# Kernel optimization log

Measured on AMD Instinct MI355X. Metric: run time of the kernel, lower is better.

Reference implementation:

```python
import jax, jax.numpy as jnp
import numpy as np

B, N, CS, CZ, H, CH, G, P = 2, 384, 384, 128, 8, 16, 2, 8
CZ4 = CZ // 4
INF = 1e5
UMAX = 3.0     # self.u_max
LMAX = 2.0     # self.log_scale_max
SQRT_CH = CH ** 0.5


def quat_to_rot(q):
    q = q / jnp.linalg.norm(q, axis=-1, keepdims=True)
    w, x, y, z = q[..., 0], q[..., 1], q[..., 2], q[..., 3]
    R = jnp.stack([
        1 - 2 * (y * y + z * z), 2 * (x * y - w * z), 2 * (x * z + w * y),
        2 * (x * y + w * z), 1 - 2 * (x * x + z * z), 2 * (y * z - w * x),
        2 * (x * z - w * y), 2 * (y * z + w * x), 1 - 2 * (x * x + y * y)], axis=-1)
    return R.reshape(q.shape[:-1] + (3, 3))


def robust_nll(delta, sigma):
    # inline robust 3x3 Cholesky solve: dist_sq = d^T S^-1 d, log_det = ln|S|
    eps = 1e-8
    s00 = sigma[..., 0, 0]; s01 = sigma[..., 0, 1]; s02 = sigma[..., 0, 2]
    s11 = sigma[..., 1, 1]; s12 = sigma[..., 1, 2]; s22 = sigma[..., 2, 2]
    d0 = delta[..., 0]; d1 = delta[..., 1]; d2 = delta[..., 2]
    l00_sq = jnp.maximum(s00, eps); inv_l00 = jax.lax.rsqrt(l00_sq)
    l10 = s01 * inv_l00; l20 = s02 * inv_l00
    l11_sq = jnp.maximum(s11 - l10 * l10, eps); inv_l11 = jax.lax.rsqrt(l11_sq)
    l21 = (s12 - l20 * l10) * inv_l11
    l22_sq = jnp.maximum(s22 - l20 * l20 - l21 * l21, eps); inv_l22 = jax.lax.rsqrt(l22_sq)
    log_det = jnp.log(l00_sq) + jnp.log(l11_sq) + jnp.log(l22_sq)
    y0 = d0 * inv_l00
    y1 = (d1 - l10 * y0) * inv_l11
    y2 = (d2 - l20 * y0 - l21 * y1) * inv_l22
    return y0 * y0 + y1 * y1 + y2 * y2, log_det


def iga_forward(s, z, mask, rot, trans, local_mean, scaling_log,
                Wq, Wk, Wv, Wb, bb, Wdz, bdz, Wqg, bqg, Wkg, bkg,
                Wvp, bvp, geo_scale, geo_bias, Wout, bout):
    # scalar q/k/v: [B,H,N,CH]
    q = (s @ Wq).reshape(B, N, H, CH).transpose(0, 2, 1, 3)
    k = (s @ Wk).reshape(B, N, H, CH).transpose(0, 2, 1, 3)
    v = (s @ Wv).reshape(B, N, H, CH).transpose(0, 2, 1, 3)
    logits = jnp.einsum('bhid,bhjd->bhij', q, k) / SQRT_CH
    # pair bias: [B,H,N,N]
    logits = logits + (z @ Wb + bb).transpose(0, 3, 1, 2)

    def parse(feat):  # -> u [B,N,H,G,3], s_log_delta [B,N,H,G,3]
        raw = feat.reshape(B, N, H, G, 6)
        return jnp.tanh(raw[..., :3]) * UMAX, jnp.tanh(raw[..., 3:]) * LMAX

    def to_global(u, sld):
        anchor = local_mean[:, :, None, None, :]
        base = scaling_log[:, :, None, None, :]
        sig_loc = jnp.maximum(jnp.exp(base + sld), 1e-6)
        pos = anchor + u * sig_loc
        mu = jnp.einsum('bnij,bnhgj->bnhgi', rot, pos) + trans[:, :, None, None, :]
        var = jnp.exp(2.0 * (base + sld))
        Sig = jnp.einsum('bnij,bnhgj,bnkj->bnhgik', rot, var, rot)  # R diag(var) R^T
        return mu.transpose(0, 2, 1, 3, 4), Sig.transpose(0, 2, 1, 3, 4, 5)

    qu, qs = parse(s @ Wqg + bqg)
    ku, ks = parse(s @ Wkg + bkg)
    q_mu, q_sig = to_global(qu, qs)   # [B,H,N,G,3], [B,H,N,G,3,3]
    k_mu, k_sig = to_global(ku, ks)
    delta = q_mu[:, :, :, None] - k_mu[:, :, None, :]      # [B,H,N,N,G,3]
    ssum = q_sig[:, :, :, None] + k_sig[:, :, None, :]     # [B,H,N,N,G,3,3]
    dist_sq, log_det = robust_nll(delta, ssum)
    geo = (-0.5 * dist_sq - 0.5 * log_det).sum(-1)          # [B,H,N,N]

    mask2d = mask[:, None, :, None] * mask[:, None, None, :]  # [B,1,N,N]
    a = jax.nn.softplus(geo_scale)[None, :, None, None]
    G_geo = a * (geo * mask2d) + geo_bias[None, :, None, None]
    logits = logits + G_geo + (1.0 - mask2d) * (-INF)
    w = jax.nn.softmax(logits, axis=-1)                      # [B,H,N,N]

    # scalar output
    o = jnp.einsum('bhij,bhjd->bihd', w, v).reshape(B, N, H * CH)
    # point output (IPA-style): to global, attend, back to local frame
    vpts = (s @ Wvp + bvp).reshape(B, N, H, P, 3)
    vpg = jnp.einsum('bnij,bnhpj->bnhpi', rot, vpts) + trans[:, :, None, None, :]
    vpg = vpg.transpose(0, 2, 1, 3, 4)                       # [B,H,N,P,3]
    opt = jnp.einsum('bhij,bhjpc->bhipc', w, vpg)            # [B,H,N,P,3]
    opt_local = jnp.einsum('bnji,bhnpj->bnhpi', rot, opt - trans[:, None, :, None, :])
    onorm = jnp.sqrt((opt_local ** 2).sum(-1) + 1e-8)        # [B,N,H,P]
    # pair output
    pz = z @ Wdz + bdz                                       # [B,N,N,CZ4]
    opair = jnp.einsum('bhij,bijc->bihc', w, pz)             # [B,N,H,CZ4]

    cat = jnp.concatenate([o, opt_local.reshape(B, N, H * P * 3),
                           onorm.reshape(B, N, H * P),
                           opair.reshape(B, N, H * CZ4)], axis=-1)  # [B,N,640]
    return cat @ Wout + bout


def setup_inputs() -> dict:
    ks = jax.random.split(jax.random.key(0), 24)
    rnd = lambda i, shape, sc=1.0: jax.random.normal(ks[i], shape, dtype=jnp.float32) * sc
    w = 0.02
    return dict(
        s=rnd(0, (B, N, CS)), z=rnd(1, (B, N, N, CZ)),
        mask=jnp.ones((B, N), jnp.float32),
        rot=quat_to_rot(rnd(2, (B, N, 4))),
        trans=rnd(3, (B, N, 3), 1.0),
        local_mean=rnd(4, (B, N, 3), 0.5),
        scaling_log=rnd(5, (B, N, 3), 0.1),
        Wq=rnd(6, (CS, H * CH), w), Wk=rnd(7, (CS, H * CH), w), Wv=rnd(8, (CS, H * CH), w),
        Wb=rnd(9, (CZ, H), w), bb=rnd(10, (H,), w),
        Wdz=rnd(11, (CZ, CZ4), w), bdz=rnd(12, (CZ4,), w),
        Wqg=rnd(13, (CS, H * G * 6), w), bqg=rnd(14, (H * G * 6,), w),
        Wkg=rnd(15, (CS, H * G * 6), w), bkg=rnd(16, (H * G * 6,), w),
        Wvp=rnd(17, (CS, H * P * 3), w), bvp=rnd(18, (H * P * 3,), w),
        geo_scale=jnp.ones((H,), jnp.float32), geo_bias=jnp.zeros((H,), jnp.float32),
        Wout=rnd(19, (H * (CH + P * 4 + CZ4), CS), w), bout=jnp.zeros((CS,), jnp.float32))


def reference(s, z, mask, rot, trans, local_mean, scaling_log, Wq, Wk, Wv, Wb, bb,
              Wdz, bdz, Wqg, bqg, Wkg, bkg, Wvp, bvp, geo_scale, geo_bias, Wout, bout):
    return iga_forward(s, z, mask, rot, trans, local_mean, scaling_log, Wq, Wk, Wv,
                       Wb, bb, Wdz, bdz, Wqg, bqg, Wkg, bkg, Wvp, bvp,
                       geo_scale, geo_bias, Wout, bout)
```

## Files before the change

kernel.cpp:

```cpp
#include <hip/hip_runtime.h>
#include <hip/hip_fp16.h>

#define NB   2
#define NN   384
#define NCS  384
#define NCZ  128
#define NH   8
#define NCH  16
#define NG   2
#define NP   8
#define NCZ4 32
#define BN   (NB*NN)
#define LINW 768

typedef _Float16 f16x8 __attribute__((ext_vector_type(8)));
typedef float    f32x4 __attribute__((ext_vector_type(4)));

__global__ void k_wprep(const float* __restrict__ Wb, const float* __restrict__ Wdz,
                        _Float16* __restrict__ wf) {
    int t = threadIdx.x;
    for (int e = t; e < 12*64*8; e += 256) {
        int r = e & 7, lane = (e >> 3) & 63, nk = e >> 9;
        int n = nk >> 2, kk = nk & 3;
        int c = kk*32 + (lane >> 4)*8 + r;
        int col = n*16 + (lane & 15);
        float w;
        if      (col < 8)  w = Wb[c*NH + col];
        else if (col < 40) w = Wdz[c*NCZ4 + (col-8)];
        else               w = 0.f;
        wf[e] = (_Float16)w;
    }
}

__global__ void k_rowlin(const float* __restrict__ s,
                         const float* __restrict__ Wq, const float* __restrict__ Wk,
                         const float* __restrict__ Wv,
                         const float* __restrict__ Wqg, const float* __restrict__ bqg,
                         const float* __restrict__ Wkg, const float* __restrict__ bkg,
                         const float* __restrict__ Wvp, const float* __restrict__ bvp,
                         float* __restrict__ lin) {
    __shared__ float sl[4][NCS];
    int t  = threadIdx.x;
    int r0 = blockIdx.x * 4;
    for (int idx = t; idx < 4*NCS; idx += 256)
        sl[idx / NCS][idx % NCS] = s[(size_t)(r0 + idx/NCS)*NCS + (idx % NCS)];
    __syncthreads();
    int col = blockIdx.y * 256 + t;
    const float* W; int sw; float bias = 0.f;
    if      (col < 128) { W = Wq  + col;        sw = 128; }
    else if (col < 256) { W = Wk  + (col-128);  sw = 128; }
    else if (col < 384) { W = Wv  + (col-256);  sw = 128; }
    else if (col < 480) { W = Wqg + (col-384);  sw = 96;  bias = bqg[col-384]; }
    else if (col < 576) { W = Wkg + (col-480);  sw = 96;  bias = bkg[col-480]; }
    else                { W = Wvp + (col-576);  sw = 192; bias = bvp[col-576]; }
    float a0=0.f, a1=0.f, a2=0.f, a3=0.f;
    for (int c = 0; c < NCS; ++c) {
        float w = W[(size_t)c*sw];
        a0 = fmaf(sl[0][c], w, a0);
        a1 = fmaf(sl[1][c], w, a1);
        a2 = fmaf(sl[2][c], w, a2);
        a3 = fmaf(sl[3][c], w, a3);
    }
    lin[(size_t)(r0+0)*LINW + col] = a0 + bias;
    lin[(size_t)(r0+1)*LINW + col] = a1 + bias;
    lin[(size_t)(r0+2)*LINW + col] = a2 + bias;
    lin[(size_t)(r0+3)*LINW + col] = a3 + bias;
}

__global__ void k_geom(const float* __restrict__ lin, const float* __restrict__ rot,
                       const float* __restrict__ trans, const float* __restrict__ lm,
                       const float* __restrict__ sc,
                       float* __restrict__ qmu, float* __restrict__ qsig,
                       float* __restrict__ kmu, float* __restrict__ ksig,
                       float* __restrict__ vpg) {
    int bn = blockIdx.x, t = threadIdx.x;
    __shared__ float R[9], T[3], A[3], Bs[3];
    if (t < 9) R[t] = rot[bn*9 + t];
    if (t < 3) { T[t] = trans[bn*3+t]; A[t] = lm[bn*3+t]; Bs[t] = sc[bn*3+t]; }
    __syncthreads();
    {
        int h = t >> 3, p = t & 7;
        const float* vr = lin + (size_t)bn*LINW + 576 + h*24 + p*3;
        float x = vr[0], y = vr[1], z = vr[2];
        float* d = vpg + (size_t)bn*(NH*NP*3) + h*24 + p*3;
        d[0] = R[0]*x + R[1]*y + R[2]*z + T[0];
        d[1] = R[3]*x + R[4]*y + R[5]*z + T[1];
        d[2] = R[6]*x + R[7]*y + R[8]*z + T[2];
    }
    if (t < 32) {
        int side = t >> 4, item = t & 15;
        const float* raw = lin + (size_t)bn*LINW + (side ? 480 : 384) + item*6;
        float u0 = tanhf(raw[0])*3.f, u1 = tanhf(raw[1])*3.f, u2 = tanhf(raw[2])*3.f;
        float e0 = Bs[0] + tanhf(raw[3])*2.f;
        float e1 = Bs[1] + tanhf(raw[4])*2.f;
        float e2 = Bs[2] + tanhf(raw[5])*2.f;
        float sl0 = fmaxf(expf(e0), 1e-6f);
        float sl1 = fmaxf(expf(e1), 1e-6f);
        float sl2 = fmaxf(expf(e2), 1e-6f);
        float p0 = A[0] + u0*sl0, p1 = A[1] + u1*sl1, p2 = A[2] + u2*sl2;
        float mu0 = R[0]*p0 + R[1]*p1 + R[2]*p2 + T[0];
        float mu1 = R[3]*p0 + R[4]*p1 + R[5]*p2 + T[1];
        float mu2 = R[6]*p0 + R[7]*p1 + R[8]*p2 + T[2];
        float v0 = expf(2.f*e0), v1 = expf(2.f*e1), v2 = expf(2.f*e2);
        float s00 = R[0]*R[0]*v0 + R[1]*R[1]*v1 + R[2]*R[2]*v2;
        float s01 = R[0]*R[3]*v0 + R[1]*R[4]*v1 + R[2]*R[5]*v2;
        float s02 = R[0]*R[6]*v0 + R[1]*R[7]*v1 + R[2]*R[8]*v2;
        float s11 = R[3]*R[3]*v0 + R[4]*R[4]*v1 + R[5]*R[5]*v2;
        float s12 = R[3]*R[6]*v0 + R[4]*R[7]*v1 + R[5]*R[8]*v2;
        float s22 = R[6]*R[6]*v0 + R[7]*R[7]*v1 + R[8]*R[8]*v2;
        float* mud = (side ? kmu : qmu) + (size_t)bn*48 + item*3;
        mud[0]=mu0; mud[1]=mu1; mud[2]=mu2;
        float* sgd = (side ? ksig : qsig) + (size_t)bn*96 + item*6;
        sgd[0]=s00; sgd[1]=s01; sgd[2]=s02; sgd[3]=s11; sgd[4]=s12; sgd[5]=s22;
    }
}

__global__ void __launch_bounds__(256, 2)
k_attn(const float* __restrict__ z, const float* __restrict__ mask,
       const float* __restrict__ rot, const float* __restrict__ trans,
       const float* __restrict__ lin,
       const float* __restrict__ qmu, const float* __restrict__ qsig,
       const float* __restrict__ kmu, const float* __restrict__ ksig,
       const float* __restrict__ vpg, const _Float16* __restrict__ wf,
       const float* __restrict__ bb, const float* __restrict__ bdz,
       const float* __restrict__ gsc, const float* __restrict__ gbi,
       float* __restrict__ cat) {
    __shared__ __align__(16) _Float16 zh[64*128];
    __shared__ float  logits[NH][NN];
    __shared__ __half pzl[NN][34];
    __shared__ float  qrow[128];
    __shared__ float  qmu_s[48], qsig_s[96];
    __shared__ float  Rm[9], Tv[3];
    __shared__ float  aH[NH], bH[NH];
    __shared__ float  bias_s[48];
    __shared__ float  maskI;

    int t  = threadIdx.x;
    int lane = t & 63, w = t >> 6;
    int b  = blockIdx.x / NN, i = blockIdx.x % NN;
    int bi = b*NN + i;
    const float* zbase = z + (size_t)bi*NN*NCZ;

    const float* zrow0 = zbase + (size_t)(t >> 5)*NCZ + (t & 31)*4;
    float4 preA[8], preB[8];
    #pragma unroll
    for (int p = 0; p < 8; ++p) preA[p] = *(const float4*)(zrow0 + (size_t)(p*8)*NCZ);
    #pragma unroll
    for (int p = 0; p < 8; ++p) preB[p] = *(const float4*)(zrow0 + (size_t)(64 + p*8)*NCZ);

    f16x8 bfr[12];
    #pragma unroll
    for (int nk = 0; nk < 12; ++nk)
        bfr[nk] = ((const f16x8*)wf)[nk*64 + lane];

    if (t < 128) qrow[t] = lin[(size_t)bi*LINW + t];
    if (t < 48)  qmu_s[t] = qmu[(size_t)bi*48 + t];
    if (t < 48)  bias_s[t] = (t < 8) ? bb[t] : ((t < 40) ? bdz[t-8] : 0.f);
    if (t >= 64 && t < 160) qsig_s[t-64] = qsig[(size_t)bi*96 + (t-64)];
    if (t >= 160 && t < 169) Rm[t-160] = rot[bi*9 + (t-160)];
    if (t >= 169 && t < 172) Tv[t-169] = trans[bi*3 + (t-169)];
    if (t >= 176 && t < 184) {
        int h = t-176;
        float x = gsc[h];
        aH[h] = (x > 20.f) ? x : log1pf(expf(x));
        bH[h] = gbi[h];
    }
    if (t == 255) maskI = mask[bi];
    __syncthreads();

    {
        int h = t >> 5, lnn = t & 31;
        float qv[16];
        #pragma unroll
        for (int d = 0; d < 16; ++d) qv[d] = qrow[h*16 + d];
        float qm[6], qs[12];
        #pragma unroll
        for (int e = 0; e < 6; ++e)  qm[e] = qmu_s[h*6 + e];
        #pragma unroll
        for (int e = 0; e < 12; ++e) qs[e] = qsig_s[h*12 + e];
        float ascale = aH[h], hbias = bH[h], mI = maskI;
        for (int jj = 0; jj < 12; ++jj) {
            int j = lnn + jj*32;
            size_t jrow = (size_t)(b*NN + j);
            const float* kp = lin + jrow*LINW + 128 + h*NCH;
            float4 k0 = *(const float4*)(kp);
            float4 k1 = *(const float4*)(kp+4);
            float4 k2 = *(const float4*)(kp+8);
            float4 k3 = *(const float4*)(kp+12);
            float qk = qv[0]*k0.x + qv[1]*k0.y + qv[2]*k0.z + qv[3]*k0.w
                     + qv[4]*k1.x + qv[5]*k1.y + qv[6]*k1.z + qv[7]*k1.w
                     + qv[8]*k2.x + qv[9]*k2.y + qv[10]*k2.z + qv[11]*k2.w
                     + qv[12]*k3.x + qv[13]*k3.y + qv[14]*k3.z + qv[15]*k3.w;
            float geo = 0.f;
            #pragma unroll
            for (int g = 0; g < NG; ++g) {
                const float* km = kmu + jrow*48 + h*6 + g*3;
                const float* ks = ksig + jrow*96 + h*12 + g*6;
                float d0 = qm[g*3+0] - km[0];
                float d1 = qm[g*3+1] - km[1];
                float d2 = qm[g*3+2] - km[2];
                float s00 = qs[g*6+0] + ks[0];
                float s01 = qs[g*6+1] + ks[1];
                float s02 = qs[g*6+2] + ks[2];
                float s11 = qs[g*6+3] + ks[3];
                float s12 = qs[g*6+4] + ks[4];
                float s22 = qs[g*6+5] + ks[5];
                float l00 = fmaxf(s00, 1e-8f);
                float i00 = rsqrtf(l00);
                float l10 = s01*i00, l20 = s02*i00;
                float l11 = fmaxf(s11 - l10*l10, 1e-8f);
                float i11 = rsqrtf(l11);
                float l21 = (s12 - l20*l10)*i11;
                float l22 = fmaxf(s22 - l20*l20 - l21*l21, 1e-8f);
                float i22 = rsqrtf(l22);
                float ld = __logf(l00) + __logf(l11) + __logf(l22);
                float y0 = d0*i00;
                float y1 = (d1 - l10*y0)*i11;
                float y2 = (d2 - l20*y0 - l21*y1)*i22;
                geo += -0.5f*(y0*y0 + y1*y1 + y2*y2 + ld);
            }
            float m2 = mI * mask[b*NN + j];
            logits[h][j] = qk*0.25f + ascale*(geo*m2) + hbias + (1.f - m2)*(-100000.f);
        }
    }

    int srow0 = t >> 5;
    int scb   = (t & 31) * 8;
    int sswz  = (srow0 & 7) << 4;
    int arow  = w*16 + (lane & 15);
    int abase = arow*256 + ((lane >> 4) << 4);
    int akey  = (lane & 7) << 4;
    int ccol  = lane & 15;
    int cjl   = w*16 + (lane >> 4)*4;

#define CHUNK_BODY(CH, PRE)                                                          \
    {                                                                                \
                              \
        _Pragma("unroll")                                                            \
        for (int p = 0; p < 8; ++p) {                                                \
            union { _Float16 h[4]; unsigned long long u; } pk;                       \
            pk.h[0] = (_Float16)PRE[p].x; pk.h[1] = (_Float16)PRE[p].y;              \
            pk.h[2] = (_Float16)PRE[p].z; pk.h[3] = (_Float16)PRE[p].w;              \
            *(unsigned long long*)((char*)zh + (p*8 + srow0)*256 + (scb ^ sswz)) = pk.u; \
        }                                                                            \
        if ((CH) + 2 < 6) {         \
            const float* src = zbase + (size_t)((CH+2)*64)*NCZ + (size_t)(t>>5)*NCZ  \
                               + (t & 31)*4;                                         \
            _Pragma("unroll")                                                        \
            for (int p = 0; p < 8; ++p)                                              \
                PRE[p] = *(const float4*)(src + (size_t)(p*8)*NCZ);                  \
        }                                                                            \
        __syncthreads();                                                             \
        {                                                                            \
            f16x8 af0 = *(const f16x8*)((const char*)zh + ((abase +   0) ^ akey));   \
            f16x8 af1 = *(const f16x8*)((const char*)zh + ((abase +  64) ^ akey));   \
            f16x8 af2 = *(const f16x8*)((const char*)zh + ((abase + 128) ^ akey));   \
            f16x8 af3 = *(const f16x8*)((const char*)zh + ((abase + 192) ^ akey));   \
            f32x4 ac0 = {0.f,0.f,0.f,0.f}, ac1 = ac0, ac2 = ac0;                     \
            ac0 = __builtin_amdgcn_mfma_f32_16x16x32_f16(af0, bfr[0], ac0, 0,0,0);   \
            ac1 = __builtin_amdgcn_mfma_f32_16x16x32_f16(af0, bfr[4], ac1, 0,0,0);   \
            ac2 = __builtin_amdgcn_mfma_f32_16x16x32_f16(af0, bfr[8], ac2, 0,0,0);   \
            ac0 = __builtin_amdgcn_mfma_f32_16x16x32_f16(af1, bfr[1], ac0, 0,0,0);   \
            ac1 = __builtin_amdgcn_mfma_f32_16x16x32_f16(af1, bfr[5], ac1, 0,0,0);   \
            ac2 = __builtin_amdgcn_mfma_f32_16x16x32_f16(af1, bfr[9], ac2, 0,0,0);   \
            ac0 = __builtin_amdgcn_mfma_f32_16x16x32_f16(af2, bfr[2], ac0, 0,0,0);   \
            ac1 = __builtin_amdgcn_mfma_f32_16x16x32_f16(af2, bfr[6], ac1, 0,0,0);   \
            ac2 = __builtin_amdgcn_mfma_f32_16x16x32_f16(af2, bfr[10], ac2, 0,0,0);  \
            ac0 = __builtin_amdgcn_mfma_f32_16x16x32_f16(af3, bfr[3], ac0, 0,0,0);   \
            ac1 = __builtin_amdgcn_mfma_f32_16x16x32_f16(af3, bfr[7], ac1, 0,0,0);   \
            ac2 = __builtin_amdgcn_mfma_f32_16x16x32_f16(af3, bfr[11], ac2, 0,0,0);  \
            int jg = (CH)*64 + cjl;                                                  \
            _Pragma("unroll")                                                        \
            for (int r = 0; r < 4; ++r) {                                            \
                int j = jg + r;                                                      \
                float v0 = ac0[r] + bias_s[ccol];                                    \
                if (ccol < 8) logits[ccol][j] += v0;                                 \
                else          pzl[j][ccol-8] = __float2half(v0);                     \
                pzl[j][ccol+8] = __float2half(ac1[r] + bias_s[16+ccol]);             \
                if (ccol < 8)                                                        \
                    pzl[j][ccol+24] = __float2half(ac2[r] + bias_s[32+ccol]);        \
            }                                                                        \
        }                                                                            \
        __syncthreads();                                                             \
    }

    CHUNK_BODY(0, preA)
    CHUNK_BODY(1, preB)
    CHUNK_BODY(2, preA)
    CHUNK_BODY(3, preB)
    CHUNK_BODY(4, preA)
    CHUNK_BODY(5, preB)
#undef CHUNK_BODY

    int h = t >> 5, lnn = t & 31;
    float mx = -3.4e38f;
    #pragma unroll
    for (int jj = 0; jj < 12; ++jj) mx = fmaxf(mx, logits[h][lnn + jj*32]);
    #pragma unroll
    for (int m = 16; m >= 1; m >>= 1) mx = fmaxf(mx, __shfl_xor(mx, m, 64));
    float se = 0.f;
    #pragma unroll
    for (int jj = 0; jj < 12; ++jj) {
        int j = lnn + jj*32;
        float e = __expf(logits[h][j] - mx);
        logits[h][j] = e;
        se += e;
    }
    #pragma unroll
    for (int m = 16; m >= 1; m >>= 1) se += __shfl_xor(se, m, 64);
    float inv = 1.f / se;

    float o[16], op[24], opa[32];
    #pragma unroll
    for (int d = 0; d < 16; ++d) o[d] = 0.f;
    #pragma unroll
    for (int e = 0; e < 24; ++e) op[e] = 0.f;
    #pragma unroll
    for (int c = 0; c < 32; ++c) opa[c] = 0.f;

    for (int jj = 0; jj < 12; ++jj) {
        int j = lnn + jj*32;
        float wgt = logits[h][j] * inv;
        size_t jrow = (size_t)(b*NN + j);
        const float* vp = lin + jrow*LINW + 256 + h*NCH;
        float vv[16];
        *reinterpret_cast<float4*>(&vv[0])  = *(const float4*)(vp);
        *reinterpret_cast<float4*>(&vv[4])  = *(const float4*)(vp+4);
        *reinterpret_cast<float4*>(&vv[8])  = *(const float4*)(vp+8);
        *reinterpret_cast<float4*>(&vv[12]) = *(const float4*)(vp+12);
        #pragma unroll
        for (int d = 0; d < 16; ++d) o[d] = fmaf(wgt, vv[d], o[d]);
        const float* vg = vpg + jrow*(NH*NP*3) + h*24;
        float gg[24];
        #pragma unroll
        for (int q4 = 0; q4 < 6; ++q4)
            *reinterpret_cast<float4*>(&gg[q4*4]) = *(const float4*)(vg + q4*4);
        #pragma unroll
        for (int e = 0; e < 24; ++e) op[e] = fmaf(wgt, gg[e], op[e]);
        const __half2* pzp = reinterpret_cast<const __half2*>(&pzl[j][0]);
        #pragma unroll
        for (int c2 = 0; c2 < 16; ++c2) {
            float2 pf = __half22float2(pzp[c2]);
            opa[2*c2]   = fmaf(wgt, pf.x, opa[2*c2]);
            opa[2*c2+1] = fmaf(wgt, pf.y, opa[2*c2+1]);
        }
    }
    #pragma unroll
    for (int m = 16; m >= 1; m >>= 1) {
        #pragma unroll
        for (int d = 0; d < 16; ++d) o[d] += __shfl_xor(o[d], m, 64);
        #pragma unroll
        for (int e = 0; e < 24; ++e) op[e] += __shfl_xor(op[e], m, 64);
        #pragma unroll
        for (int c = 0; c < 32; ++c) opa[c] += __shfl_xor(opa[c], m, 64);
    }
    if (lnn == 0) {
        float* cp = cat + (size_t)bi*640;
        #pragma unroll
        for (int d = 0; d < 16; ++d) cp[h*16 + d] = o[d];
        #pragma unroll
        for (int p = 0; p < 8; ++p) {
            float x  = op[p*3+0] - Tv[0];
            float y  = op[p*3+1] - Tv[1];
            float zz = op[p*3+2] - Tv[2];
            float l0 = Rm[0]*x + Rm[3]*y + Rm[6]*zz;
            float l1 = Rm[1]*x + Rm[4]*y + Rm[7]*zz;
            float l2 = Rm[2]*x + Rm[5]*y + Rm[8]*zz;
            cp[128 + h*24 + p*3 + 0] = l0;
            cp[128 + h*24 + p*3 + 1] = l1;
            cp[128 + h*24 + p*3 + 2] = l2;
            cp[320 + h*8 + p] = sqrtf(l0*l0 + l1*l1 + l2*l2 + 1e-8f);
        }
        #pragma unroll
        for (int c = 0; c < 32; ++c) cp[384 + h*32 + c] = opa[c];
    }
}

__global__ void k_out(const float* __restrict__ cat, const float* __restrict__ Wout,
                      const float* __restrict__ bout, float* __restrict__ out) {
    __shared__ float cl[4][640];
    int t  = threadIdx.x;
    int r0 = blockIdx.x * 4;
    for (int idx = t; idx < 4*640; idx += 384)
        cl[idx/640][idx%640] = cat[(size_t)(r0 + idx/640)*640 + (idx%640)];
    __syncthreads();
    int col = t;
    float a0=0.f, a1=0.f, a2=0.f, a3=0.f;
    for (int c = 0; c < 640; ++c) {
        float w = Wout[(size_t)c*NCS + col];
        a0 = fmaf(cl[0][c], w, a0);
        a1 = fmaf(cl[1][c], w, a1);
        a2 = fmaf(cl[2][c], w, a2);
        a3 = fmaf(cl[3][c], w, a3);
    }
    float bv = bout[col];
    out[(size_t)(r0+0)*NCS + col] = a0 + bv;
    out[(size_t)(r0+1)*NCS + col] = a1 + bv;
    out[(size_t)(r0+2)*NCS + col] = a2 + bv;
    out[(size_t)(r0+3)*NCS + col] = a3 + bv;
}

extern "C" void kernel_launch(void* const* d_in, const int* in_sizes, int n_in,
                              void* d_out, int out_size, void* d_ws, size_t ws_size,
                              hipStream_t stream) {
    const float* s    = (const float*)d_in[0];
    const float* z    = (const float*)d_in[1];
    const float* mask = (const float*)d_in[2];
    const float* rot  = (const float*)d_in[3];
    const float* trans= (const float*)d_in[4];
    const float* lm   = (const float*)d_in[5];
    const float* sc   = (const float*)d_in[6];
    const float* Wq   = (const float*)d_in[7];
    const float* Wk   = (const float*)d_in[8];
    const float* Wv   = (const float*)d_in[9];
    const float* Wb   = (const float*)d_in[10];
    const float* bb   = (const float*)d_in[11];
    const float* Wdz  = (const float*)d_in[12];
    const float* bdz  = (const float*)d_in[13];
    const float* Wqg  = (const float*)d_in[14];
    const float* bqg  = (const float*)d_in[15];
    const float* Wkg  = (const float*)d_in[16];
    const float* bkg  = (const float*)d_in[17];
    const float* Wvp  = (const float*)d_in[18];
    const float* bvp  = (const float*)d_in[19];
    const float* gsc  = (const float*)d_in[20];
    const float* gbi  = (const float*)d_in[21];
    const float* Wout = (const float*)d_in[22];
    const float* bout = (const float*)d_in[23];
    float* out = (float*)d_out;

    float* ws   = (float*)d_ws;
    float* lin  = ws;
    float* qmu  = lin  + 589824;
    float* qsig = qmu  + 36864;
    float* kmu  = qsig + 73728;
    float* ksig = kmu  + 36864;
    float* vpg  = ksig + 73728;
    float* cat  = vpg  + 147456;
    _Float16* wf = (_Float16*)(cat + 491520);

    k_wprep<<<1, 256, 0, stream>>>(Wb, Wdz, wf);
    k_rowlin<<<dim3(192, 3), 256, 0, stream>>>(s, Wq, Wk, Wv, Wqg, bqg, Wkg, bkg,
                                               Wvp, bvp, lin);
    k_geom<<<BN, 64, 0, stream>>>(lin, rot, trans, lm, sc, qmu, qsig, kmu, ksig, vpg);
    k_attn<<<BN, 256, 0, stream>>>(z, mask, rot, trans, lin, qmu, qsig, kmu, ksig,
                                   vpg, wf, bb, bdz, gsc, gbi, cat);
    k_out<<<192, 384, 0, stream>>>(cat, Wout, bout, out);
}
```

Measured before the change: 180.1 us.

## Transpose key-side tensors to feature-major layout for coalesced attention loads

```diff
diff --git a/kernel.cpp b/kernel.cpp
--- a/kernel.cpp
+++ b/kernel.cpp
@@ -38,7 +38,8 @@
                          const float* __restrict__ Wqg, const float* __restrict__ bqg,
                          const float* __restrict__ Wkg, const float* __restrict__ bkg,
                          const float* __restrict__ Wvp, const float* __restrict__ bvp,
-                         float* __restrict__ lin) {
+                         float* __restrict__ lin,
+                         float* __restrict__ kT, float* __restrict__ vT) {
     __shared__ float sl[4][NCS];
     int t  = threadIdx.x;
     int r0 = blockIdx.x * 4;
@@ -65,14 +66,20 @@
     lin[(size_t)(r0+1)*LINW + col] = a1 + bias;
     lin[(size_t)(r0+2)*LINW + col] = a2 + bias;
     lin[(size_t)(r0+3)*LINW + col] = a3 + bias;
+    if (col >= 128 && col < 384) {
+        f32x4 v4; v4[0]=a0; v4[1]=a1; v4[2]=a2; v4[3]=a3;
+        float* dst = (col < 256) ? (kT + (size_t)(col-128)*BN + r0)
+                                 : (vT + (size_t)(col-256)*BN + r0);
+        *(f32x4*)dst = v4;
+    }
 }
 
 __global__ void k_geom(const float* __restrict__ lin, const float* __restrict__ rot,
                        const float* __restrict__ trans, const float* __restrict__ lm,
                        const float* __restrict__ sc,
                        float* __restrict__ qmu, float* __restrict__ qsig,
-                       float* __restrict__ kmu, float* __restrict__ ksig,
-                       float* __restrict__ vpg) {
+                       float* __restrict__ kmuT, float* __restrict__ ksigT,
+                       float* __restrict__ vpgT) {
     int bn = blockIdx.x, t = threadIdx.x;
     __shared__ float R[9], T[3], A[3], Bs[3];
     if (t < 9) R[t] = rot[bn*9 + t];
@@ -82,10 +89,10 @@
         int h = t >> 3, p = t & 7;
         const float* vr = lin + (size_t)bn*LINW + 576 + h*24 + p*3;
         float x = vr[0], y = vr[1], z = vr[2];
-        float* d = vpg + (size_t)bn*(NH*NP*3) + h*24 + p*3;
-        d[0] = R[0]*x + R[1]*y + R[2]*z + T[0];
-        d[1] = R[3]*x + R[4]*y + R[5]*z + T[1];
-        d[2] = R[6]*x + R[7]*y + R[8]*z + T[2];
+        int e = h*24 + p*3;
+        vpgT[(size_t)(e+0)*BN + bn] = R[0]*x + R[1]*y + R[2]*z + T[0];
+        vpgT[(size_t)(e+1)*BN + bn] = R[3]*x + R[4]*y + R[5]*z + T[1];
+        vpgT[(size_t)(e+2)*BN + bn] = R[6]*x + R[7]*y + R[8]*z + T[2];
     }
     if (t < 32) {
         int side = t >> 4, item = t & 15;
@@ -108,10 +115,22 @@
         float s11 = R[3]*R[3]*v0 + R[4]*R[4]*v1 + R[5]*R[5]*v2;
         float s12 = R[3]*R[6]*v0 + R[4]*R[7]*v1 + R[5]*R[8]*v2;
         float s22 = R[6]*R[6]*v0 + R[7]*R[7]*v1 + R[8]*R[8]*v2;
-        float* mud = (side ? kmu : qmu) + (size_t)bn*48 + item*3;
-        mud[0]=mu0; mud[1]=mu1; mud[2]=mu2;
-        float* sgd = (side ? ksig : qsig) + (size_t)bn*96 + item*6;
-        sgd[0]=s00; sgd[1]=s01; sgd[2]=s02; sgd[3]=s11; sgd[4]=s12; sgd[5]=s22;
+        if (side) {
+            kmuT[(size_t)(item*3+0)*BN + bn] = mu0;
+            kmuT[(size_t)(item*3+1)*BN + bn] = mu1;
+            kmuT[(size_t)(item*3+2)*BN + bn] = mu2;
+            ksigT[(size_t)(item*6+0)*BN + bn] = s00;
+            ksigT[(size_t)(item*6+1)*BN + bn] = s01;
+            ksigT[(size_t)(item*6+2)*BN + bn] = s02;
+            ksigT[(size_t)(item*6+3)*BN + bn] = s11;
+            ksigT[(size_t)(item*6+4)*BN + bn] = s12;
+            ksigT[(size_t)(item*6+5)*BN + bn] = s22;
+        } else {
+            float* mud = qmu + (size_t)bn*48 + item*3;
+            mud[0]=mu0; mud[1]=mu1; mud[2]=mu2;
+            float* sgd = qsig + (size_t)bn*96 + item*6;
+            sgd[0]=s00; sgd[1]=s01; sgd[2]=s02; sgd[3]=s11; sgd[4]=s12; sgd[5]=s22;
+        }
     }
 }
 
@@ -120,8 +139,9 @@
        const float* __restrict__ rot, const float* __restrict__ trans,
        const float* __restrict__ lin,
        const float* __restrict__ qmu, const float* __restrict__ qsig,
-       const float* __restrict__ kmu, const float* __restrict__ ksig,
-       const float* __restrict__ vpg, const _Float16* __restrict__ wf,
+       const float* __restrict__ kmuT, const float* __restrict__ ksigT,
+       const float* __restrict__ kT, const float* __restrict__ vT,
+       const float* __restrict__ vpgT, const _Float16* __restrict__ wf,
        const float* __restrict__ bb, const float* __restrict__ bdz,
        const float* __restrict__ gsc, const float* __restrict__ gbi,
        float* __restrict__ cat) {
@@ -140,6 +160,7 @@
     int b  = blockIdx.x / NN, i = blockIdx.x % NN;
     int bi = b*NN + i;
     const float* zbase = z + (size_t)bi*NN*NCZ;
+    const size_t boff = (size_t)b*NN;
 
     const float* zrow0 = zbase + (size_t)(t >> 5)*NCZ + (t & 31)*4;
     float4 preA[8], preB[8];
@@ -147,11 +168,6 @@
     for (int p = 0; p < 8; ++p) preA[p] = *(const float4*)(zrow0 + (size_t)(p*8)*NCZ);
     #pragma unroll
     for (int p = 0; p < 8; ++p) preB[p] = *(const float4*)(zrow0 + (size_t)(64 + p*8)*NCZ);
-
-    f16x8 bfr[12];
-    #pragma unroll
-    for (int nk = 0; nk < 12; ++nk)
-        bfr[nk] = ((const f16x8*)wf)[nk*64 + lane];
 
     if (t < 128) qrow[t] = lin[(size_t)bi*LINW + t];
     if (t < 48)  qmu_s[t] = qmu[(size_t)bi*48 + t];
@@ -179,50 +195,72 @@
         #pragma unroll
         for (int e = 0; e < 12; ++e) qs[e] = qsig_s[h*12 + e];
         float ascale = aH[h], hbias = bH[h], mI = maskI;
-        for (int jj = 0; jj < 12; ++jj) {
-            int j = lnn + jj*32;
-            size_t jrow = (size_t)(b*NN + j);
-            const float* kp = lin + jrow*LINW + 128 + h*NCH;
-            float4 k0 = *(const float4*)(kp);
-            float4 k1 = *(const float4*)(kp+4);
-            float4 k2 = *(const float4*)(kp+8);
-            float4 k3 = *(const float4*)(kp+12);
-            float qk = qv[0]*k0.x + qv[1]*k0.y + qv[2]*k0.z + qv[3]*k0.w
-                     + qv[4]*k1.x + qv[5]*k1.y + qv[6]*k1.z + qv[7]*k1.w
-                     + qv[8]*k2.x + qv[9]*k2.y + qv[10]*k2.z + qv[11]*k2.w
-                     + qv[12]*k3.x + qv[13]*k3.y + qv[14]*k3.z + qv[15]*k3.w;
-            float geo = 0.f;
+        #pragma unroll 1
+        for (int jj = 0; jj < 3; ++jj) {
+            int j4 = jj*128 + lnn*4;
+            const float* kp = kT + (size_t)(h*16)*BN + boff + j4;
+            f32x4 qk = {0.f,0.f,0.f,0.f};
+            #pragma unroll
+            for (int d = 0; d < 16; ++d) {
+                f32x4 kv = *(const f32x4*)(kp + (size_t)d*BN);
+                #pragma unroll
+                for (int r = 0; r < 4; ++r) qk[r] = fmaf(qv[d], kv[r], qk[r]);
+            }
+            f32x4 geo = {0.f,0.f,0.f,0.f};
             #pragma unroll
             for (int g = 0; g < NG; ++g) {
-                const float* km = kmu + jrow*48 + h*6 + g*3;
-                const float* ks = ksig + jrow*96 + h*12 + g*6;
-                float d0 = qm[g*3+0] - km[0];
-                float d1 = qm[g*3+1] - km[1];
-                float d2 = qm[g*3+2] - km[2];
-                float s00 = qs[g*6+0] + ks[0];
-                float s01 = qs[g*6+1] + ks[1];
-                float s02 = qs[g*6+2] + ks[2];
-                float s11 = qs[g*6+3] + ks[3];
-                float s12 = qs[g*6+4] + ks[4];
-                float s22 = qs[g*6+5] + ks[5];
-                float l00 = fmaxf(s00, 1e-8f);
-                float i00 = rsqrtf(l00);
-                float l10 = s01*i00, l20 = s02*i00;
-                float l11 = fmaxf(s11 - l10*l10, 1e-8f);
-                float i11 = rsqrtf(l11);
-                float l21 = (s12 - l20*l10)*i11;
-                float l22 = fmaxf(s22 - l20*l20 - l21*l21, 1e-8f);
-                float i22 = rsqrtf(l22);
-                float ld = __logf(l00) + __logf(l11) + __logf(l22);
-                float y0 = d0*i00;
-                float y1 = (d1 - l10*y0)*i11;
-                float y2 = (d2 - l20*y0 - l21*y1)*i22;
-                geo += -0.5f*(y0*y0 + y1*y1 + y2*y2 + ld);
+                const float* kmb = kmuT + (size_t)((h*2+g)*3)*BN + boff + j4;
+                f32x4 km0 = *(const f32x4*)(kmb);
+                f32x4 km1 = *(const f32x4*)(kmb + BN);
+                f32x4 km2 = *(const f32x4*)(kmb + 2*BN);
+                const float* ksb = ksigT + (size_t)((h*2+g)*6)*BN + boff + j4;
+                f32x4 ks0 = *(const f32x4*)(ksb);
+                f32x4 ks1 = *(const f32x4*)(ksb + BN);
+                f32x4 ks2 = *(const f32x4*)(ksb + 2*BN);
+                f32x4 ks3 = *(const f32x4*)(ksb + 3*BN);
+                f32x4 ks4 = *(const f32x4*)(ksb + 4*BN);
+                f32x4 ks5 = *(const f32x4*)(ksb + 5*BN);
+                #pragma unroll
+                for (int r = 0; r < 4; ++r) {
+                    float d0 = qm[g*3+0] - km0[r];
+                    float d1 = qm[g*3+1] - km1[r];
+                    float d2 = qm[g*3+2] - km2[r];
+                    float s00 = qs[g*6+0] + ks0[r];
+                    float s01 = qs[g*6+1] + ks1[r];
+                    float s02 = qs[g*6+2] + ks2[r];
+                    float s11 = qs[g*6+3] + ks3[r];
+                    float s12 = qs[g*6+4] + ks4[r];
+                    float s22 = qs[g*6+5] + ks5[r];
+                    float l00 = fmaxf(s00, 1e-8f);
+                    float i00 = rsqrtf(l00);
+                    float l10 = s01*i00, l20 = s02*i00;
+                    float l11 = fmaxf(s11 - l10*l10, 1e-8f);
+                    float i11 = rsqrtf(l11);
+                    float l21 = (s12 - l20*l10)*i11;
+                    float l22 = fmaxf(s22 - l20*l20 - l21*l21, 1e-8f);
+                    float i22 = rsqrtf(l22);
+                    float ld = __logf(l00) + __logf(l11) + __logf(l22);
+                    float y0 = d0*i00;
+                    float y1 = (d1 - l10*y0)*i11;
+                    float y2 = (d2 - l20*y0 - l21*y1)*i22;
+                    geo[r] += -0.5f*(y0*y0 + y1*y1 + y2*y2 + ld);
+                }
             }
-            float m2 = mI * mask[b*NN + j];
-            logits[h][j] = qk*0.25f + ascale*(geo*m2) + hbias + (1.f - m2)*(-100000.f);
+            f32x4 mv = *(const f32x4*)(mask + boff + j4);
+            f32x4 lg;
+            #pragma unroll
+            for (int r = 0; r < 4; ++r) {
+                float m2 = mI * mv[r];
+                lg[r] = qk[r]*0.25f + ascale*(geo[r]*m2) + hbias + (1.f - m2)*(-100000.f);
+            }
+            *(f32x4*)&logits[h][j4] = lg;
         }
     }
+
+    f16x8 bfr[12];
+    #pragma unroll
+    for (int nk = 0; nk < 12; ++nk)
+        bfr[nk] = ((const f16x8*)wf)[nk*64 + lane];
 
     int srow0 = t >> 5;
     int scb   = (t & 31) * 8;
@@ -235,7 +273,6 @@
 
 #define CHUNK_BODY(CH, PRE)                                                          \
     {                                                                                \
-                              \
         _Pragma("unroll")                                                            \
         for (int p = 0; p < 8; ++p) {                                                \
             union { _Float16 h[4]; unsigned long long u; } pk;                       \
@@ -243,7 +280,7 @@
             pk.h[2] = (_Float16)PRE[p].z; pk.h[3] = (_Float16)PRE[p].w;              \
             *(unsigned long long*)((char*)zh + (p*8 + srow0)*256 + (scb ^ sswz)) = pk.u; \
         }                                                                            \
-        if ((CH) + 2 < 6) {         \
+        if ((CH) + 2 < 6) {                                                          \
             const float* src = zbase + (size_t)((CH+2)*64)*NCZ + (size_t)(t>>5)*NCZ  \
                                + (t & 31)*4;                                         \
             _Pragma("unroll")                                                        \
@@ -318,25 +355,18 @@
     #pragma unroll
     for (int c = 0; c < 32; ++c) opa[c] = 0.f;
 
+    const float* vbase = vT + (size_t)(h*16)*BN + boff + lnn;
+    const float* gbase = vpgT + (size_t)(h*24)*BN + boff + lnn;
+    #pragma unroll 1
     for (int jj = 0; jj < 12; ++jj) {
         int j = lnn + jj*32;
         float wgt = logits[h][j] * inv;
-        size_t jrow = (size_t)(b*NN + j);
-        const float* vp = lin + jrow*LINW + 256 + h*NCH;
-        float vv[16];
-        *reinterpret_cast<float4*>(&vv[0])  = *(const float4*)(vp);
-        *reinterpret_cast<float4*>(&vv[4])  = *(const float4*)(vp+4);
-        *reinterpret_cast<float4*>(&vv[8])  = *(const float4*)(vp+8);
-        *reinterpret_cast<float4*>(&vv[12]) = *(const float4*)(vp+12);
-        #pragma unroll
-        for (int d = 0; d < 16; ++d) o[d] = fmaf(wgt, vv[d], o[d]);
-        const float* vg = vpg + jrow*(NH*NP*3) + h*24;
-        float gg[24];
-        #pragma unroll
-        for (int q4 = 0; q4 < 6; ++q4)
-            *reinterpret_cast<float4*>(&gg[q4*4]) = *(const float4*)(vg + q4*4);
-        #pragma unroll
-        for (int e = 0; e < 24; ++e) op[e] = fmaf(wgt, gg[e], op[e]);
+        const float* vb = vbase + jj*32;
+        #pragma unroll
+        for (int d = 0; d < 16; ++d) o[d] = fmaf(wgt, vb[(size_t)d*BN], o[d]);
+        const float* gb = gbase + jj*32;
+        #pragma unroll
+        for (int e = 0; e < 24; ++e) op[e] = fmaf(wgt, gb[(size_t)e*BN], op[e]);
         const __half2* pzp = reinterpret_cast<const __half2*>(&pzl[j][0]);
         #pragma unroll
         for (int c2 = 0; c2 < 16; ++c2) {
@@ -429,21 +459,23 @@
     const float* bout = (const float*)d_in[23];
     float* out = (float*)d_out;
 
-    float* ws   = (float*)d_ws;
-    float* lin  = ws;
-    float* qmu  = lin  + 589824;
-    float* qsig = qmu  + 36864;
-    float* kmu  = qsig + 73728;
-    float* ksig = kmu  + 36864;
-    float* vpg  = ksig + 73728;
-    float* cat  = vpg  + 147456;
+    float* ws    = (float*)d_ws;
+    float* lin   = ws;
+    float* qmu   = lin   + 589824;
+    float* qsig  = qmu   + 36864;
+    float* kmuT  = qsig  + 73728;
+    float* ksigT = kmuT  + 36864;
+    float* vpgT  = ksigT + 73728;
+    float* kT    = vpgT  + 147456;
+    float* vT    = kT    + 98304;
+    float* cat   = vT    + 98304;
     _Float16* wf = (_Float16*)(cat + 491520);
 
     k_wprep<<<1, 256, 0, stream>>>(Wb, Wdz, wf);
     k_rowlin<<<dim3(192, 3), 256, 0, stream>>>(s, Wq, Wk, Wv, Wqg, bqg, Wkg, bkg,
-                                               Wvp, bvp, lin);
-    k_geom<<<BN, 64, 0, stream>>>(lin, rot, trans, lm, sc, qmu, qsig, kmu, ksig, vpg);
-    k_attn<<<BN, 256, 0, stream>>>(z, mask, rot, trans, lin, qmu, qsig, kmu, ksig,
-                                   vpg, wf, bb, bdz, gsc, gbi, cat);
+                                               Wvp, bvp, lin, kT, vT);
+    k_geom<<<BN, 64, 0, stream>>>(lin, rot, trans, lm, sc, qmu, qsig, kmuT, ksigT, vpgT);
+    k_attn<<<BN, 256, 0, stream>>>(z, mask, rot, trans, lin, qmu, qsig, kmuT, ksigT,
+                                   kT, vT, vpgT, wf, bb, bdz, gsc, gbi, cat);
     k_out<<<192, 384, 0, stream>>>(cat, Wout, bout, out);
 }
```

After: 158.5 us. -12.0%, faster.
